# Kernel tuning notes

Measured on AMD Instinct MI355X. Metric: run time of the kernel, lower is better.

Reference implementation:

```python
import jax, jax.numpy as jnp
import numpy as np

B, M, K, N = 4, 2048, 4096, 4096


def setup_inputs() -> dict:
    key = jax.random.key(0)
    k1, k2, k3, k4, k5 = jax.random.split(key, 5)
    # int8 quantized activations and weights (stored as int8, like the torch buffers)
    x_q = jax.random.randint(k1, (B, M, K), -128, 127, dtype=jnp.int8)
    weight = jax.random.randint(k2, (N, K), -128, 127, dtype=jnp.int8)
    # per-token activation scales and per-output-row weight scales (symmetric quant)
    scales_x = jax.random.uniform(k3, (B, M, 1), dtype=jnp.float32) * 0.01 + 1e-4
    weight_scales = jax.random.uniform(k4, (N, 1), dtype=jnp.float32) * 0.01 + 1e-4
    bias = jax.random.normal(k5, (N,), dtype=jnp.float32)
    return {"x_q": x_q, "scales_x": scales_x, "weight": weight,
            "weight_scales": weight_scales, "bias": bias}


def reference(x_q, scales_x, weight, weight_scales, bias):
    # int8 GEMM accumulating in int32: (B*M, K) @ (K, N) with weight stored (N, K)
    acc = jnp.einsum(
        'bmk,nk->bmn',
        x_q.astype(jnp.int32), weight.astype(jnp.int32),
        preferred_element_type=jnp.int32,
    )  # [B, M, N] int32
    # symmetric dequant: row (token) scale * column (output-channel) scale, then bias
    out = acc.astype(jnp.float32) * scales_x * weight_scales[:, 0] + bias
    return out.astype(jnp.float16)
```

## Files before the change

### kernel.cpp

```cpp
#include <hip/hip_runtime.h>

typedef int v4i __attribute__((ext_vector_type(4)));

constexpr int Kdim = 4096;
constexpr int Ndim = 4096;
constexpr int MtotC = 8192;
constexpr int BM = 256;
constexpr int BN = 256;
constexpr int BKB = 128;
constexpr int NT = Kdim / BKB;

__global__ void pack_i32_to_i8(const int* __restrict__ xq, const int* __restrict__ wq,
                               signed char* __restrict__ x8, signed char* __restrict__ w8,
                               size_t nx4, size_t nw4) {
    size_t i = (size_t)blockIdx.x * blockDim.x + threadIdx.x;
    size_t stride = (size_t)gridDim.x * blockDim.x;
    size_t tot = nx4 + nw4;
    for (size_t j = i; j < tot; j += stride) {
        if (j < nx4) {
            const int4 v = ((const int4*)xq)[j];
            char4 c;
            c.x = (signed char)v.x; c.y = (signed char)v.y;
            c.z = (signed char)v.z; c.w = (signed char)v.w;
            ((char4*)x8)[j] = c;
        } else {
            const size_t k = j - nx4;
            const int4 v = ((const int4*)wq)[k];
            char4 c;
            c.x = (signed char)v.x; c.y = (signed char)v.y;
            c.z = (signed char)v.z; c.w = (signed char)v.w;
            ((char4*)w8)[k] = c;
        }
    }
}

__global__ __launch_bounds__(512, 2) void i8gemm_kernel(
    const signed char* __restrict__ A,
    const signed char* __restrict__ W,
    const float* __restrict__ sx,
    const float* __restrict__ wsc,
    const float* __restrict__ bias,
    float* __restrict__ C)
{
    extern __shared__ signed char smem[];

    const int tid  = threadIdx.x;
    const int wave = tid >> 6;
    const int lane = tid & 63;
    const int wr = wave >> 2;
    const int wc = wave & 3;

    const int xr_ = blockIdx.x & 7;
    const int idx = blockIdx.x >> 3;
    const int bm = ((xr_ & 3) * 8 + (idx & 7)) * BM;
    const int bn = ((xr_ >> 2) * 8 + (idx >> 3)) * BN;

    const int srow_in = wave * 16 + (lane >> 2);
    const int sslotp  = lane & 3;
    const int gslot   = sslotp ^ ((srow_in >> 1) & 3);
    const signed char* Ag = A + (size_t)(bm + srow_in) * Kdim + gslot * 16;
    const signed char* Wg = W + (size_t)(bn + srow_in) * Kdim + gslot * 16;
    const int sdst = srow_in * 64 + sslotp * 16;

    const int frow = lane & 15;
    const int fsl  = lane >> 4;
    const int rsw  = ((fsl ^ ((frow >> 1) & 3)) << 4);
    const int aro  = (wr * 128 + frow) * 64 + rsw;
    const int bro  = 16384 + (wc * 64 + frow) * 64 + rsw;

    v4i acc[8][4];
#pragma unroll
    for (int f = 0; f < 8; ++f)
#pragma unroll
        for (int g = 0; g < 4; ++g)
#pragma unroll
            for (int e = 0; e < 4; ++e) acc[f][g][e] = 0;

#define STG(KT, HALF, RB) do {                                                         \
    __builtin_amdgcn_global_load_lds(                                                  \
        (const __attribute__((address_space(1))) void*)(Ag + (size_t)(RB) * Kdim + (KT) * BKB + (HALF) * 64), \
        (__attribute__((address_space(3))) void*)(smem + ((KT) & 1) * 65536 + (HALF) * 32768 + (RB) * 64 + sdst), \
        16, 0, 0);                                                                     \
    __builtin_amdgcn_global_load_lds(                                                  \
        (const __attribute__((address_space(1))) void*)(Wg + (size_t)(RB) * Kdim + (KT) * BKB + (HALF) * 64), \
        (__attribute__((address_space(3))) void*)(smem + ((KT) & 1) * 65536 + (HALF) * 32768 + 16384 + (RB) * 64 + sdst), \
        16, 0, 0);                                                                     \
} while (0)

#define BAR   __builtin_amdgcn_s_barrier()
#define LGKM0 asm volatile("s_waitcnt lgkmcnt(0)" ::: "memory")
#define PRIO1 __builtin_amdgcn_s_setprio(1)
#define PRIO0 __builtin_amdgcn_s_setprio(0)

#define PH_READ_AB(HALF) do {                                                          \
    _Pragma("unroll") for (int g_ = 0; g_ < 4; ++g_)                                   \
        bv[g_] = *(const v4i*)(bufb + (HALF) * 32768 + bro + g_ * 1024);               \
    _Pragma("unroll") for (int f_ = 0; f_ < 4; ++f_)                                   \
        av[f_] = *(const v4i*)(bufb + (HALF) * 32768 + aro + f_ * 1024);               \
} while (0)

#define PH_READ_A4(HALF) do {                                                          \
    _Pragma("unroll") for (int f_ = 0; f_ < 4; ++f_)                                   \
        av[f_] = *(const v4i*)(bufb + (HALF) * 32768 + aro + (4 + f_) * 1024);         \
} while (0)

#define MFMA_BLOCK(FB) do {                                                            \
    _Pragma("unroll") for (int f_ = 0; f_ < 4; ++f_)                                   \
    _Pragma("unroll") for (int g_ = 0; g_ < 4; ++g_)                                   \
        acc[(FB) + f_][g_] = __builtin_amdgcn_mfma_i32_16x16x64_i8(                    \
            av[f_], bv[g_], acc[(FB) + f_][g_], 0, 0, 0);                              \
} while (0)

#define TILE_BODY(U, DOS12, DOS34, W2STR, DOW4, W4STR) do {                            \
    signed char* bufb = smem + ((U) & 1) * 65536;                                      \
    v4i av[4], bv[4];                                                                  \
                                                        \
    PH_READ_AB(0);                                                                     \
    if (DOS12) STG((U) + 1, 1, 0);                                                     \
    BAR; LGKM0; PRIO1; MFMA_BLOCK(0); PRIO0; BAR;                                      \
                                                        \
    PH_READ_A4(0);                                                                     \
    if (DOS12) STG((U) + 1, 1, 128);                                                   \
    BAR; LGKM0; PRIO1; MFMA_BLOCK(4); PRIO0;                                           \
    asm volatile("s_waitcnt " W2STR ::: "memory"); BAR;                                \
                                                        \
    PH_READ_AB(1);                                                                     \
    if (DOS34) STG((U) + 2, 0, 0);                                                     \
    BAR; LGKM0; PRIO1; MFMA_BLOCK(0); PRIO0; BAR;                                      \
                                                        \
    PH_READ_A4(1);                                                                     \
    if (DOS34) STG((U) + 2, 0, 128);                                                   \
    BAR; LGKM0; PRIO1; MFMA_BLOCK(4); PRIO0;                                           \
    if (DOW4) { asm volatile("s_waitcnt " W4STR ::: "memory"); }                       \
    BAR;                                                                               \
} while (0)

    STG(0, 0, 0);  STG(0, 0, 128);
    STG(0, 1, 0);  STG(0, 1, 128);
    STG(1, 0, 0);  STG(1, 0, 128);
    asm volatile("s_waitcnt vmcnt(8)" ::: "memory");
    BAR;

    for (int u = 0; u < NT - 2; ++u)
        TILE_BODY(u, true, true, "vmcnt(8)", true, "vmcnt(8)");
    TILE_BODY(NT - 2, true,  false, "vmcnt(8)", true,  "vmcnt(4)");
    TILE_BODY(NT - 1, false, false, "vmcnt(0)", false, "vmcnt(0)");

    const int orow0 = bm + wr * 128;
    const int ocol0 = bn + wc * 64;
    float wsv[4], bvv[4];
#pragma unroll
    for (int g = 0; g < 4; ++g) {
        const int col = ocol0 + g * 16 + frow;
        wsv[g] = wsc[col];
        bvv[g] = bias[col];
    }
#pragma unroll
    for (int f = 0; f < 8; ++f) {
#pragma unroll
        for (int jr = 0; jr < 4; ++jr) {
            const int row = orow0 + f * 16 + fsl * 4 + jr;
            const float s = sx[row];
#pragma unroll
            for (int g = 0; g < 4; ++g) {
                const int col = ocol0 + g * 16 + frow;
                C[(size_t)row * Ndim + col] = (float)acc[f][g][jr] * s * wsv[g] + bvv[g];
            }
        }
    }
#undef STG
#undef BAR
#undef LGKM0
#undef PRIO1
#undef PRIO0
#undef PH_READ_AB
#undef PH_READ_A4
#undef MFMA_BLOCK
#undef TILE_BODY
}

extern "C" void kernel_launch(void* const* d_in, const int* in_sizes, int n_in,
                              void* d_out, int out_size, void* d_ws, size_t ws_size,
                              hipStream_t stream) {
    (void)in_sizes; (void)n_in; (void)out_size; (void)ws_size;
    const int*   x_q  = (const int*)d_in[0];
    const float* sx   = (const float*)d_in[1];
    const int*   w_q  = (const int*)d_in[2];
    const float* wsc  = (const float*)d_in[3];
    const float* bias = (const float*)d_in[4];
    float* out = (float*)d_out;

    signed char* x8 = (signed char*)d_ws;
    signed char* w8 = x8 + (size_t)MtotC * Kdim;

    const size_t nx = (size_t)MtotC * Kdim;
    const size_t nw = (size_t)Ndim * Kdim;

    pack_i32_to_i8<<<3072, 256, 0, stream>>>(x_q, w_q, x8, w8, nx / 4, nw / 4);

    static bool attr_set = false;
    if (!attr_set) {
        hipFuncSetAttribute((const void*)i8gemm_kernel,
                            hipFuncAttributeMaxDynamicSharedMemorySize, 131072);
        attr_set = true;
    }

    const int nwg = (MtotC / BM) * (Ndim / BN);
    i8gemm_kernel<<<nwg, 512, 131072, stream>>>(x8, w8, sx, wsc, bias, out);
}
```

Measured before the change: 189.5 us.

## Switch int8 GEMM to 32x32x32 MFMA tiles and drop pre-MFMA barriers

Replaces the 16x16x64 i8 MFMA fragments with 32x32x32 i8 MFMA, changing the accumulator layout to 4x2 blocks of 16 ints and rewriting the LDS fragment reads and epilogue index mapping to match. Each phase now issues 8 larger MFMAs instead of 16 small ones, which reduces LDS read traffic per FLOP and instruction count. It also removes the barrier that came before each MFMA block, cutting synchronization. This relies on the new swizzle offsets matching the staging layout, and removing barriers risks races if LDS buffer reuse was depending on them.

```diff
diff --git a/kernel.cpp b/kernel.cpp
--- a/kernel.cpp
+++ b/kernel.cpp
@@ -1,6 +1,7 @@
 #include <hip/hip_runtime.h>
 
-typedef int v4i __attribute__((ext_vector_type(4)));
+typedef int v4i  __attribute__((ext_vector_type(4)));
+typedef int v16i __attribute__((ext_vector_type(16)));
 
 constexpr int Kdim = 4096;
 constexpr int Ndim = 4096;
@@ -62,19 +63,21 @@
     const signed char* Wg = W + (size_t)(bn + srow_in) * Kdim + gslot * 16;
     const int sdst = srow_in * 64 + sslotp * 16;
 
-    const int frow = lane & 15;
-    const int fsl  = lane >> 4;
-    const int rsw  = ((fsl ^ ((frow >> 1) & 3)) << 4);
-    const int aro  = (wr * 128 + frow) * 64 + rsw;
-    const int bro  = 16384 + (wc * 64 + frow) * 64 + rsw;
-
-    v4i acc[8][4];
-#pragma unroll
-    for (int f = 0; f < 8; ++f)
-#pragma unroll
-        for (int g = 0; g < 4; ++g)
-#pragma unroll
-            for (int e = 0; e < 4; ++e) acc[f][g][e] = 0;
+    const int l31 = lane & 31;
+    const int hi  = lane >> 5;
+    const int xm  = (l31 >> 1) & 3;
+    const int ps0 = ((hi)     ^ xm) * 16;
+    const int ps1 = ((2 + hi) ^ xm) * 16;
+    const int aro = (wr * 128 + l31) * 64;
+    const int bro = 16384 + (wc * 64 + l31) * 64;
+
+    v16i acc[4][2];
+#pragma unroll
+    for (int f = 0; f < 4; ++f)
+#pragma unroll
+        for (int g = 0; g < 2; ++g)
+#pragma unroll
+            for (int e = 0; e < 16; ++e) acc[f][g][e] = 0;
 
 #define STG(KT, HALF, RB) do {                                                         \
     __builtin_amdgcn_global_load_lds(                                                  \
@@ -93,46 +96,55 @@
 #define PRIO0 __builtin_amdgcn_s_setprio(0)
 
 #define PH_READ_AB(HALF) do {                                                          \
-    _Pragma("unroll") for (int g_ = 0; g_ < 4; ++g_)                                   \
-        bv[g_] = *(const v4i*)(bufb + (HALF) * 32768 + bro + g_ * 1024);               \
-    _Pragma("unroll") for (int f_ = 0; f_ < 4; ++f_)                                   \
-        av[f_] = *(const v4i*)(bufb + (HALF) * 32768 + aro + f_ * 1024);               \
-} while (0)
-
-#define PH_READ_A4(HALF) do {                                                          \
-    _Pragma("unroll") for (int f_ = 0; f_ < 4; ++f_)                                   \
-        av[f_] = *(const v4i*)(bufb + (HALF) * 32768 + aro + (4 + f_) * 1024);         \
-} while (0)
-
-#define MFMA_BLOCK(FB) do {                                                            \
-    _Pragma("unroll") for (int f_ = 0; f_ < 4; ++f_)                                   \
-    _Pragma("unroll") for (int g_ = 0; g_ < 4; ++g_)                                   \
-        acc[(FB) + f_][g_] = __builtin_amdgcn_mfma_i32_16x16x64_i8(                    \
-            av[f_], bv[g_], acc[(FB) + f_][g_], 0, 0, 0);                              \
-} while (0)
-
-#define TILE_BODY(U, DOS12, DOS34, W2STR, DOW4, W4STR) do {                            \
+    bv[0] = *(const v4i*)(bufb + (HALF) * 32768 + bro +    0 + ps0);                   \
+    bv[1] = *(const v4i*)(bufb + (HALF) * 32768 + bro + 2048 + ps0);                   \
+    bv[2] = *(const v4i*)(bufb + (HALF) * 32768 + bro +    0 + ps1);                   \
+    bv[3] = *(const v4i*)(bufb + (HALF) * 32768 + bro + 2048 + ps1);                   \
+    av[0] = *(const v4i*)(bufb + (HALF) * 32768 + aro +    0 + ps0);                   \
+    av[1] = *(const v4i*)(bufb + (HALF) * 32768 + aro + 2048 + ps0);                   \
+    av[2] = *(const v4i*)(bufb + (HALF) * 32768 + aro +    0 + ps1);                   \
+    av[3] = *(const v4i*)(bufb + (HALF) * 32768 + aro + 2048 + ps1);                   \
+} while (0)
+
+#define PH_READ_A2(HALF) do {                                                          \
+    av[0] = *(const v4i*)(bufb + (HALF) * 32768 + aro + 4096 + ps0);                   \
+    av[1] = *(const v4i*)(bufb + (HALF) * 32768 + aro + 6144 + ps0);                   \
+    av[2] = *(const v4i*)(bufb + (HALF) * 32768 + aro + 4096 + ps1);                   \
+    av[3] = *(const v4i*)(bufb + (HALF) * 32768 + aro + 6144 + ps1);                   \
+} while (0)
+
+#define MFMA8(RB) do {                                                                 \
+    acc[RB][0]     = __builtin_amdgcn_mfma_i32_32x32x32_i8(av[0], bv[0], acc[RB][0], 0, 0, 0);     \
+    acc[RB + 1][0] = __builtin_amdgcn_mfma_i32_32x32x32_i8(av[1], bv[0], acc[RB + 1][0], 0, 0, 0); \
+    acc[RB][1]     = __builtin_amdgcn_mfma_i32_32x32x32_i8(av[0], bv[1], acc[RB][1], 0, 0, 0);     \
+    acc[RB + 1][1] = __builtin_amdgcn_mfma_i32_32x32x32_i8(av[1], bv[1], acc[RB + 1][1], 0, 0, 0); \
+    acc[RB][0]     = __builtin_amdgcn_mfma_i32_32x32x32_i8(av[2], bv[2], acc[RB][0], 0, 0, 0);     \
+    acc[RB + 1][0] = __builtin_amdgcn_mfma_i32_32x32x32_i8(av[3], bv[2], acc[RB + 1][0], 0, 0, 0); \
+    acc[RB][1]     = __builtin_amdgcn_mfma_i32_32x32x32_i8(av[2], bv[3], acc[RB][1], 0, 0, 0);     \
+    acc[RB + 1][1] = __builtin_amdgcn_mfma_i32_32x32x32_i8(av[3], bv[3], acc[RB + 1][1], 0, 0, 0); \
+} while (0)
+
+#define TILE_BODY(U, DOS12, DOS34, W2STR, W4STR) do {                                  \
     signed char* bufb = smem + ((U) & 1) * 65536;                                      \
     v4i av[4], bv[4];                                                                  \
-                                                        \
+                                                            \
     PH_READ_AB(0);                                                                     \
     if (DOS12) STG((U) + 1, 1, 0);                                                     \
-    BAR; LGKM0; PRIO1; MFMA_BLOCK(0); PRIO0; BAR;                                      \
-                                                        \
-    PH_READ_A4(0);                                                                     \
+    LGKM0; PRIO1; MFMA8(0); PRIO0; BAR;                                                \
+                                                            \
+    PH_READ_A2(0);                                                                     \
     if (DOS12) STG((U) + 1, 1, 128);                                                   \
-    BAR; LGKM0; PRIO1; MFMA_BLOCK(4); PRIO0;                                           \
+    LGKM0; PRIO1; MFMA8(2); PRIO0;                                                     \
     asm volatile("s_waitcnt " W2STR ::: "memory"); BAR;                                \
-                                                        \
+                                                            \
     PH_READ_AB(1);                                                                     \
     if (DOS34) STG((U) + 2, 0, 0);                                                     \
-    BAR; LGKM0; PRIO1; MFMA_BLOCK(0); PRIO0; BAR;                                      \
-                                                        \
-    PH_READ_A4(1);                                                                     \
+    LGKM0; PRIO1; MFMA8(0); PRIO0; BAR;                                                \
+                                                            \
+    PH_READ_A2(1);                                                                     \
     if (DOS34) STG((U) + 2, 0, 128);                                                   \
-    BAR; LGKM0; PRIO1; MFMA_BLOCK(4); PRIO0;                                           \
-    if (DOW4) { asm volatile("s_waitcnt " W4STR ::: "memory"); }                       \
-    BAR;                                                                               \
+    LGKM0; PRIO1; MFMA8(2); PRIO0;                                                     \
+    asm volatile("s_waitcnt " W4STR ::: "memory"); BAR;                                \
 } while (0)
 
     STG(0, 0, 0);  STG(0, 0, 128);
@@ -142,29 +154,23 @@
     BAR;
 
     for (int u = 0; u < NT - 2; ++u)
-        TILE_BODY(u, true, true, "vmcnt(8)", true, "vmcnt(8)");
-    TILE_BODY(NT - 2, true,  false, "vmcnt(8)", true,  "vmcnt(4)");
-    TILE_BODY(NT - 1, false, false, "vmcnt(0)", false, "vmcnt(0)");
+        TILE_BODY(u, true, true, "vmcnt(8)", "vmcnt(8)");
+    TILE_BODY(NT - 2, true,  false, "vmcnt(8)", "vmcnt(4)");
+    TILE_BODY(NT - 1, false, false, "vmcnt(0)", "vmcnt(0)");
 
     const int orow0 = bm + wr * 128;
     const int ocol0 = bn + wc * 64;
-    float wsv[4], bvv[4];
-#pragma unroll
-    for (int g = 0; g < 4; ++g) {
-        const int col = ocol0 + g * 16 + frow;
-        wsv[g] = wsc[col];
-        bvv[g] = bias[col];
-    }
-#pragma unroll
-    for (int f = 0; f < 8; ++f) {
-#pragma unroll
-        for (int jr = 0; jr < 4; ++jr) {
-            const int row = orow0 + f * 16 + fsl * 4 + jr;
-            const float s = sx[row];
-#pragma unroll
-            for (int g = 0; g < 4; ++g) {
-                const int col = ocol0 + g * 16 + frow;
-                C[(size_t)row * Ndim + col] = (float)acc[f][g][jr] * s * wsv[g] + bvv[g];
+#pragma unroll
+    for (int rb = 0; rb < 4; ++rb) {
+#pragma unroll
+        for (int cb = 0; cb < 2; ++cb) {
+            const int col = ocol0 + cb * 32 + l31;
+            const float wb = wsc[col];
+            const float bb = bias[col];
+#pragma unroll
+            for (int r = 0; r < 16; ++r) {
+                const int row = orow0 + rb * 32 + (r & 3) + 8 * (r >> 2) + 4 * hi;
+                C[(size_t)row * Ndim + col] = (float)acc[rb][cb][r] * sx[row] * wb + bb;
             }
         }
     }
@@ -174,8 +180,8 @@
 #undef PRIO1
 #undef PRIO0
 #undef PH_READ_AB
-#undef PH_READ_A4
-#undef MFMA_BLOCK
+#undef PH_READ_A2
+#undef MFMA8
 #undef TILE_BODY
 }
 
```

Result: slower. 206.7 us (+9.1%).

## Replace phased interleaved tile schedule with simple full-tile load-then-compute loop

Applied to the files above, without the earlier changes.

Replaces the four-phase per-tile schedule, which interleaved half-tile global->LDS staging with LDS reads and MFMA blocks under barriers and s_setprio, with a plain loop. Each iteration now reads the whole tile's A/B fragments from LDS into registers, issues all 64 MFMAs, then stages the tile two steps ahead and waits. This drops many barriers and priority toggles, and lets the compiler schedule LDS reads and MFMAs freely. In exchange it keeps more fragments live in registers, and global loads are now issued only after compute, so load/compute overlap is reduced.

```diff
diff --git a/kernel.cpp b/kernel.cpp
--- a/kernel.cpp
+++ b/kernel.cpp
@@ -87,64 +87,53 @@
         16, 0, 0);                                                                     \
 } while (0)
 
-#define BAR   __builtin_amdgcn_s_barrier()
-#define LGKM0 asm volatile("s_waitcnt lgkmcnt(0)" ::: "memory")
-#define PRIO1 __builtin_amdgcn_s_setprio(1)
-#define PRIO0 __builtin_amdgcn_s_setprio(0)
-
-#define PH_READ_AB(HALF) do {                                                          \
-    _Pragma("unroll") for (int g_ = 0; g_ < 4; ++g_)                                   \
-        bv[g_] = *(const v4i*)(bufb + (HALF) * 32768 + bro + g_ * 1024);               \
-    _Pragma("unroll") for (int f_ = 0; f_ < 4; ++f_)                                   \
-        av[f_] = *(const v4i*)(bufb + (HALF) * 32768 + aro + f_ * 1024);               \
+#define STAGEFULL(KT) do {                                                             \
+    STG(KT, 0, 0);  STG(KT, 0, 128);                                                   \
+    STG(KT, 1, 0);  STG(KT, 1, 128);                                                   \
 } while (0)
 
-#define PH_READ_A4(HALF) do {                                                          \
-    _Pragma("unroll") for (int f_ = 0; f_ < 4; ++f_)                                   \
-        av[f_] = *(const v4i*)(bufb + (HALF) * 32768 + aro + (4 + f_) * 1024);         \
-} while (0)
+#define BAR __builtin_amdgcn_s_barrier()
 
-#define MFMA_BLOCK(FB) do {                                                            \
-    _Pragma("unroll") for (int f_ = 0; f_ < 4; ++f_)                                   \
-    _Pragma("unroll") for (int g_ = 0; g_ < 4; ++g_)                                   \
-        acc[(FB) + f_][g_] = __builtin_amdgcn_mfma_i32_16x16x64_i8(                    \
-            av[f_], bv[g_], acc[(FB) + f_][g_], 0, 0, 0);                              \
-} while (0)
-
-#define TILE_BODY(U, DOS12, DOS34, W2STR, DOW4, W4STR) do {                            \
-    signed char* bufb = smem + ((U) & 1) * 65536;                                      \
-    v4i av[4], bv[4];                                                                  \
-                                                        \
-    PH_READ_AB(0);                                                                     \
-    if (DOS12) STG((U) + 1, 1, 0);                                                     \
-    BAR; LGKM0; PRIO1; MFMA_BLOCK(0); PRIO0; BAR;                                      \
-                                                        \
-    PH_READ_A4(0);                                                                     \
-    if (DOS12) STG((U) + 1, 1, 128);                                                   \
-    BAR; LGKM0; PRIO1; MFMA_BLOCK(4); PRIO0;                                           \
-    asm volatile("s_waitcnt " W2STR ::: "memory"); BAR;                                \
-                                                        \
-    PH_READ_AB(1);                                                                     \
-    if (DOS34) STG((U) + 2, 0, 0);                                                     \
-    BAR; LGKM0; PRIO1; MFMA_BLOCK(0); PRIO0; BAR;                                      \
-                                                        \
-    PH_READ_A4(1);                                                                     \
-    if (DOS34) STG((U) + 2, 0, 128);                                                   \
-    BAR; LGKM0; PRIO1; MFMA_BLOCK(4); PRIO0;                                           \
-    if (DOW4) { asm volatile("s_waitcnt " W4STR ::: "memory"); }                       \
-    BAR;                                                                               \
-} while (0)
-
-    STG(0, 0, 0);  STG(0, 0, 128);
-    STG(0, 1, 0);  STG(0, 1, 128);
-    STG(1, 0, 0);  STG(1, 0, 128);
+    STAGEFULL(0);
+    STAGEFULL(1);
     asm volatile("s_waitcnt vmcnt(8)" ::: "memory");
     BAR;
 
-    for (int u = 0; u < NT - 2; ++u)
-        TILE_BODY(u, true, true, "vmcnt(8)", true, "vmcnt(8)");
-    TILE_BODY(NT - 2, true,  false, "vmcnt(8)", true,  "vmcnt(4)");
-    TILE_BODY(NT - 1, false, false, "vmcnt(0)", false, "vmcnt(0)");
+    for (int u = 0; u < NT; ++u) {
+        const signed char* bufb = smem + (u & 1) * 65536;
+
+        v4i av0[8], bv0[4], av1[8], bv1[4];
+#pragma unroll
+        for (int g = 0; g < 4; ++g) bv0[g] = *(const v4i*)(bufb + bro + g * 1024);
+#pragma unroll
+        for (int f = 0; f < 8; ++f) av0[f] = *(const v4i*)(bufb + aro + f * 1024);
+#pragma unroll
+        for (int g = 0; g < 4; ++g) bv1[g] = *(const v4i*)(bufb + 32768 + bro + g * 1024);
+#pragma unroll
+        for (int f = 0; f < 8; ++f) av1[f] = *(const v4i*)(bufb + 32768 + aro + f * 1024);
+
+#pragma unroll
+        for (int f = 0; f < 8; ++f)
+#pragma unroll
+            for (int g = 0; g < 4; ++g)
+                acc[f][g] = __builtin_amdgcn_mfma_i32_16x16x64_i8(av0[f], bv0[g], acc[f][g], 0, 0, 0);
+#pragma unroll
+        for (int f = 0; f < 8; ++f)
+#pragma unroll
+            for (int g = 0; g < 4; ++g)
+                acc[f][g] = __builtin_amdgcn_mfma_i32_16x16x64_i8(av1[f], bv1[g], acc[f][g], 0, 0, 0);
+
+        BAR;
+
+        if (u + 2 < NT) {
+            STAGEFULL(u + 2);
+            asm volatile("s_waitcnt vmcnt(8)" ::: "memory");
+            BAR;
+        } else if (u + 1 < NT) {
+            asm volatile("s_waitcnt vmcnt(0)" ::: "memory");
+            BAR;
+        }
+    }
 
     const int orow0 = bm + wr * 128;
     const int ocol0 = bn + wc * 64;
@@ -169,14 +158,8 @@
         }
     }
 #undef STG
+#undef STAGEFULL
 #undef BAR
-#undef LGKM0
-#undef PRIO1
-#undef PRIO0
-#undef PH_READ_AB
-#undef PH_READ_A4
-#undef MFMA_BLOCK
-#undef TILE_BODY
 }
 
 extern "C" void kernel_launch(void* const* d_in, const int* in_sizes, int n_in,
```

New measurement: 190.6 us. About the same (+0.6%).

## Fuse activation int32-to-int8 packing into GEMM A-tile loads

Applied to the files above, without the earlier changes.

The separate pre-pass that narrowed activations from int32 to int8 is removed. The GEMM now loads int32 activations into registers, packs them to int8 with byte permutes, and stores them into LDS inside the software pipeline. Weights are still pre-packed by a smaller kernel. This avoids writing and re-reading a 32 MB int8 activation copy, but each workgroup reads 4x more activation bytes from global memory (re-read across N tiles) and spends VGPRs and VALU on the packing.

```diff
diff --git a/kernel.cpp b/kernel.cpp
--- a/kernel.cpp
+++ b/kernel.cpp
@@ -7,35 +7,25 @@
 constexpr int MtotC = 8192;
 constexpr int BM = 256;
 constexpr int BN = 256;
-constexpr int BKB = 128;
-constexpr int NT = Kdim / BKB;
-
-__global__ void pack_i32_to_i8(const int* __restrict__ xq, const int* __restrict__ wq,
-                               signed char* __restrict__ x8, signed char* __restrict__ w8,
-                               size_t nx4, size_t nw4) {
+constexpr int NT = 32;
+
+#define AS1 __attribute__((address_space(1)))
+#define AS3 __attribute__((address_space(3)))
+
+__global__ void pack_w_i8(const int* __restrict__ wq, signed char* __restrict__ w8, size_t n4) {
     size_t i = (size_t)blockIdx.x * blockDim.x + threadIdx.x;
     size_t stride = (size_t)gridDim.x * blockDim.x;
-    size_t tot = nx4 + nw4;
-    for (size_t j = i; j < tot; j += stride) {
-        if (j < nx4) {
-            const int4 v = ((const int4*)xq)[j];
-            char4 c;
-            c.x = (signed char)v.x; c.y = (signed char)v.y;
-            c.z = (signed char)v.z; c.w = (signed char)v.w;
-            ((char4*)x8)[j] = c;
-        } else {
-            const size_t k = j - nx4;
-            const int4 v = ((const int4*)wq)[k];
-            char4 c;
-            c.x = (signed char)v.x; c.y = (signed char)v.y;
-            c.z = (signed char)v.z; c.w = (signed char)v.w;
-            ((char4*)w8)[k] = c;
-        }
+    for (size_t j = i; j < n4; j += stride) {
+        const int4 v = ((const int4*)wq)[j];
+        char4 c;
+        c.x = (signed char)v.x; c.y = (signed char)v.y;
+        c.z = (signed char)v.z; c.w = (signed char)v.w;
+        ((char4*)w8)[j] = c;
     }
 }
 
 __global__ __launch_bounds__(512, 2) void i8gemm_kernel(
-    const signed char* __restrict__ A,
+    const int* __restrict__ Xq,
     const signed char* __restrict__ W,
     const float* __restrict__ sx,
     const float* __restrict__ wsc,
@@ -58,7 +48,7 @@
     const int srow_in = wave * 16 + (lane >> 2);
     const int sslotp  = lane & 3;
     const int gslot   = sslotp ^ ((srow_in >> 1) & 3);
-    const signed char* Ag = A + (size_t)(bm + srow_in) * Kdim + gslot * 16;
+    const int* Xg = Xq + (size_t)(bm + srow_in) * Kdim + gslot * 16;
     const signed char* Wg = W + (size_t)(bn + srow_in) * Kdim + gslot * 16;
     const int sdst = srow_in * 64 + sslotp * 16;
 
@@ -76,15 +66,29 @@
 #pragma unroll
             for (int e = 0; e < 4; ++e) acc[f][g][e] = 0;
 
-#define STG(KT, HALF, RB) do {                                                         \
-    __builtin_amdgcn_global_load_lds(                                                  \
-        (const __attribute__((address_space(1))) void*)(Ag + (size_t)(RB) * Kdim + (KT) * BKB + (HALF) * 64), \
-        (__attribute__((address_space(3))) void*)(smem + ((KT) & 1) * 65536 + (HALF) * 32768 + (RB) * 64 + sdst), \
-        16, 0, 0);                                                                     \
-    __builtin_amdgcn_global_load_lds(                                                  \
-        (const __attribute__((address_space(1))) void*)(Wg + (size_t)(RB) * Kdim + (KT) * BKB + (HALF) * 64), \
-        (__attribute__((address_space(3))) void*)(smem + ((KT) & 1) * 65536 + (HALF) * 32768 + 16384 + (RB) * 64 + sdst), \
-        16, 0, 0);                                                                     \
+    v4i astA[4], astB[4];
+
+#define AISS(SET, KT, HALF, R) do {                                                    \
+    _Pragma("unroll") for (int j_ = 0; j_ < 4; ++j_)                                   \
+        SET[j_] = *(const v4i*)(Xg + (size_t)((R) * 128) * Kdim                        \
+                                + (size_t)(KT) * 128 + (HALF) * 64 + j_ * 4);          \
+} while (0)
+
+#define PACKST(SET, KT, HALF, R) do {                                                  \
+    v4i wv_;                                                                           \
+    _Pragma("unroll") for (int d_ = 0; d_ < 4; ++d_) {                                 \
+        unsigned p1_ = __builtin_amdgcn_perm((unsigned)SET[d_][1], (unsigned)SET[d_][0], 0x00000400u); \
+        unsigned p2_ = __builtin_amdgcn_perm((unsigned)SET[d_][3], (unsigned)SET[d_][2], 0x00000400u); \
+        wv_[d_] = (int)__builtin_amdgcn_perm(p2_, p1_, 0x05040100u);                   \
+    }                                                                                  \
+    *(v4i*)(smem + (size_t)(((KT) & 1) * 65536 + (HALF) * 32768 + (R) * 8192 + sdst)) = wv_; \
+} while (0)
+
+#define BISS(KT, HALF) do {                                                            \
+    const signed char* sb_ = Wg + (size_t)(KT) * 128 + (HALF) * 64;                    \
+    signed char* db_ = smem + ((KT) & 1) * 65536 + (HALF) * 32768 + 16384 + sdst;      \
+    __builtin_amdgcn_global_load_lds((const AS1 void*)sb_,                        (AS3 void*)db_,          16, 0, 0); \
+    __builtin_amdgcn_global_load_lds((const AS1 void*)(sb_ + (size_t)128 * Kdim), (AS3 void*)(db_ + 8192), 16, 0, 0); \
 } while (0)
 
 #define BAR   __builtin_amdgcn_s_barrier()
@@ -111,40 +115,48 @@
             av[f_], bv[g_], acc[(FB) + f_][g_], 0, 0, 0);                              \
 } while (0)
 
-#define TILE_BODY(U, DOS12, DOS34, W2STR, DOW4, W4STR) do {                            \
-    signed char* bufb = smem + ((U) & 1) * 65536;                                      \
-    v4i av[4], bv[4];                                                                  \
-                                                        \
-    PH_READ_AB(0);                                                                     \
-    if (DOS12) STG((U) + 1, 1, 0);                                                     \
-    BAR; LGKM0; PRIO1; MFMA_BLOCK(0); PRIO0; BAR;                                      \
-                                                        \
-    PH_READ_A4(0);                                                                     \
-    if (DOS12) STG((U) + 1, 1, 128);                                                   \
-    BAR; LGKM0; PRIO1; MFMA_BLOCK(4); PRIO0;                                           \
-    asm volatile("s_waitcnt " W2STR ::: "memory"); BAR;                                \
-                                                        \
-    PH_READ_AB(1);                                                                     \
-    if (DOS34) STG((U) + 2, 0, 0);                                                     \
-    BAR; LGKM0; PRIO1; MFMA_BLOCK(0); PRIO0; BAR;                                      \
-                                                        \
-    PH_READ_A4(1);                                                                     \
-    if (DOS34) STG((U) + 2, 0, 128);                                                   \
-    BAR; LGKM0; PRIO1; MFMA_BLOCK(4); PRIO0;                                           \
-    if (DOW4) { asm volatile("s_waitcnt " W4STR ::: "memory"); }                       \
-    BAR;                                                                               \
-} while (0)
-
-    STG(0, 0, 0);  STG(0, 0, 128);
-    STG(0, 1, 0);  STG(0, 1, 128);
-    STG(1, 0, 0);  STG(1, 0, 128);
-    asm volatile("s_waitcnt vmcnt(8)" ::: "memory");
+    BISS(0, 0);
+    AISS(astA, 0, 0, 0); PACKST(astA, 0, 0, 0);
+    AISS(astA, 0, 0, 1); PACKST(astA, 0, 0, 1);
+    BISS(0, 1);
+    AISS(astA, 0, 1, 0); PACKST(astA, 0, 1, 0);
+    AISS(astA, 0, 1, 1); PACKST(astA, 0, 1, 1);
+    BISS(1, 0);
+    AISS(astA, 1, 0, 0); PACKST(astA, 1, 0, 0);
+    AISS(astB, 1, 0, 1);
+    LGKM0;
     BAR;
 
-    for (int u = 0; u < NT - 2; ++u)
-        TILE_BODY(u, true, true, "vmcnt(8)", true, "vmcnt(8)");
-    TILE_BODY(NT - 2, true,  false, "vmcnt(8)", true,  "vmcnt(4)");
-    TILE_BODY(NT - 1, false, false, "vmcnt(0)", false, "vmcnt(0)");
+    for (int u = 0; u < NT; ++u) {
+        const signed char* bufb = smem + (u & 1) * 65536;
+        v4i av[4], bv[4];
+        PH_READ_AB(0);
+        if (u < NT - 1) {
+            BISS(u + 1, 1);
+            AISS(astA, u + 1, 1, 0);
+            PACKST(astB, u + 1, 0, 1);
+        }
+        BAR; LGKM0; PRIO1; MFMA_BLOCK(0); PRIO0; BAR;
+        PH_READ_A4(0);
+        if (u < NT - 1) {
+            AISS(astB, u + 1, 1, 1);
+            PACKST(astA, u + 1, 1, 0);
+        }
+        BAR; LGKM0; PRIO1; MFMA_BLOCK(4); PRIO0; BAR;
+        PH_READ_AB(1);
+        if (u < NT - 2) {
+            BISS(u + 2, 0);
+            AISS(astA, u + 2, 0, 0);
+        }
+        if (u < NT - 1) PACKST(astB, u + 1, 1, 1);
+        BAR; LGKM0; PRIO1; MFMA_BLOCK(0); PRIO0; BAR;
+        PH_READ_A4(1);
+        if (u < NT - 2) {
+            AISS(astB, u + 2, 0, 1);
+            PACKST(astA, u + 2, 0, 0);
+        }
+        BAR; LGKM0; PRIO1; MFMA_BLOCK(4); PRIO0; BAR;
+    }
 
     const int orow0 = bm + wr * 128;
     const int ocol0 = bn + wc * 64;
@@ -168,7 +180,9 @@
             }
         }
     }
-#undef STG
+#undef AISS
+#undef PACKST
+#undef BISS
 #undef BAR
 #undef LGKM0
 #undef PRIO1
@@ -176,7 +190,6 @@
 #undef PH_READ_AB
 #undef PH_READ_A4
 #undef MFMA_BLOCK
-#undef TILE_BODY
 }
 
 extern "C" void kernel_launch(void* const* d_in, const int* in_sizes, int n_in,
@@ -190,13 +203,10 @@
     const float* bias = (const float*)d_in[4];
     float* out = (float*)d_out;
 
-    signed char* x8 = (signed char*)d_ws;
-    signed char* w8 = x8 + (size_t)MtotC * Kdim;
-
-    const size_t nx = (size_t)MtotC * Kdim;
+    signed char* w8 = (signed char*)d_ws;
     const size_t nw = (size_t)Ndim * Kdim;
 
-    pack_i32_to_i8<<<3072, 256, 0, stream>>>(x_q, w_q, x8, w8, nx / 4, nw / 4);
+    pack_w_i8<<<1024, 256, 0, stream>>>(w_q, w8, nw / 4);
 
     static bool attr_set = false;
     if (!attr_set) {
@@ -206,5 +216,5 @@
     }
 
     const int nwg = (MtotC / BM) * (Ndim / BN);
-    i8gemm_kernel<<<nwg, 512, 131072, stream>>>(x8, w8, sx, wsc, bias, out);
+    i8gemm_kernel<<<nwg, 512, 131072, stream>>>(x_q, w8, sx, wsc, bias, out);
 }
```

After: 280.1 us. 47.8% more time.
